# Kernel optimization log

Measured on AMD Instinct MI355X. Metric: run time of the kernel, lower is better.

The kernel has to match this reference:

```python
import jax, jax.numpy as jnp
import numpy as np

N = 8192          # total nodes in batch
D_IN = 64         # input feature dim
D_H = 64          # hidden dim
D_OUT = 10        # num classes
B = 64            # number of graphs (idx in [0, B))
NUM_ITERS = 5     # power iterations for rs-pool
VALUE_ALPHA = 1.0
EPS = 0.0         # GIN eps (train_eps=False)


def setup_inputs() -> dict:
    key = jax.random.key(0)
    ks = jax.random.split(key, 8)
    x_in = jax.random.normal(ks[0], (N, D_IN), dtype=jnp.float32)
    a = (jax.random.uniform(ks[1], (N, N)) < 0.005).astype(jnp.float32)
    adj = jnp.maximum(a, a.T)
    idx = (jnp.arange(N) // (N // B)).astype(jnp.int32)  # 64 graphs x 128 nodes
    s1 = 1.0 / np.sqrt(D_IN)
    s2 = 1.0 / np.sqrt(D_H)
    W1 = jax.random.uniform(ks[2], (D_IN, D_H), minval=-s1, maxval=s1, dtype=jnp.float32)
    b1 = jax.random.uniform(ks[3], (D_H,), minval=-s1, maxval=s1, dtype=jnp.float32)
    W2 = jax.random.uniform(ks[4], (D_H, D_H), minval=-s2, maxval=s2, dtype=jnp.float32)
    b2 = jax.random.uniform(ks[5], (D_H,), minval=-s2, maxval=s2, dtype=jnp.float32)
    Wl = jax.random.uniform(ks[6], (D_H, D_OUT), minval=-s2, maxval=s2, dtype=jnp.float32)
    bl = jax.random.uniform(ks[7], (D_OUT,), minval=-s2, maxval=s2, dtype=jnp.float32)
    return {"x_in": x_in, "adj": adj, "idx": idx,
            "W1": W1, "b1": b1, "W2": W2, "b2": b2, "Wl": Wl, "bl": bl}


def reference(x_in, adj, idx, W1, b1, W2, b2, Wl, bl):
    n = adj.shape[0]
    A = adj + jnp.eye(n, dtype=adj.dtype)  # self-loops added in forward
    # GINConv: aggregate (A@x + eps*x) then linear + ReLU
    h = jax.nn.relu((A @ x_in + EPS * x_in) @ W1 + b1)   # [N, D_H]
    h = jax.nn.relu((A @ h + EPS * h) @ W2 + b2)         # [N, D_H]

    seg = lambda v: jax.ops.segment_sum(v, idx, num_segments=B)

    # rs-pool: batched power iteration for dominant right singular vector per graph
    vec = seg(h)                                                   # [B, D_H]
    vec = vec / (jnp.linalg.norm(vec, axis=1, keepdims=True) + 1e-8)
    for _ in range(NUM_ITERS):
        y = jnp.sum(h * vec[idx], axis=1, keepdims=True)           # X_g @ v_g, per node
        vec = seg(y * h)                                           # X_g^T (X_g v_g)
        vec = vec / (jnp.linalg.norm(vec, axis=1, keepdims=True) + 1e-8)
    y = jnp.sum(h * vec[idx], axis=1)                              # [N]
    sv = jnp.sqrt(seg(y * y))                                      # ||X_g v_g|| per graph [B]
    pooled = vec * (sv / VALUE_ALPHA)[:, None]                     # [B, D_H]

    out = pooled @ Wl + bl                                         # [B, D_OUT]
    return jax.nn.log_softmax(out, axis=1)
```

## Files before the change

kernel.cpp:

```cpp
#include <hip/hip_runtime.h>
#include <math.h>

#define NN 8192
#define DH 64
#define DOUT 10
#define NG 64
#define NPG 128
#define NITER 5
#define CAP 192
#define NCHUNK (NN * NN / 256)
#define RPW 2

typedef float f32x4 __attribute__((ext_vector_type(4)));
typedef unsigned long long u64;
typedef u64 u64x2 __attribute__((ext_vector_type(2)));

__global__ __launch_bounds__(256) void scan_bitmap(
    const float* __restrict__ adj, u64* __restrict__ bmp)
{
    const int lane = threadIdx.x & 63;
    const int gw   = (blockIdx.x * 256 + threadIdx.x) >> 6;
    const int nw   = (gridDim.x * 256) >> 6;
    #pragma unroll 4
    for (int g = gw; g < NCHUNK; g += nw) {
        f32x4 a4 = *reinterpret_cast<const f32x4*>(adj + (size_t)g * 256 + lane * 4);
        u64 m0 = __ballot(a4.x != 0.0f);
        u64 m1 = __ballot(a4.y != 0.0f);
        u64 m2 = __ballot(a4.z != 0.0f);
        u64 m3 = __ballot(a4.w != 0.0f);
        u64 msel = (lane & 2) ? ((lane & 1) ? m3 : m2)
                              : ((lane & 1) ? m1 : m0);
        if (lane < 4) bmp[(size_t)g * 4 + lane] = msel;
    }
}

__global__ __launch_bounds__(256) void gin_layer(
    const float* __restrict__ x, const u64* __restrict__ bmp,
    const float* __restrict__ W, const float* __restrict__ bias,
    float* __restrict__ out)
{
    __shared__ float sW[DH * DH];
    __shared__ unsigned short sJ[4][CAP];

    for (int t = threadIdx.x; t < DH * DH; t += 256) sW[t] = W[t];
    __syncthreads();

    const int wave = threadIdx.x >> 6;
    const int lane = threadIdx.x & 63;

    float wreg[DH];
    #pragma unroll
    for (int k = 0; k < DH; ++k) wreg[k] = sW[k * DH + lane];
    const float bl_ = bias[lane];

    const int wgid = blockIdx.x * 4 + wave;

    for (int rr = 0; rr < RPW; ++rr) {
        const int row = wgid * RPW + rr;
        const u64* brow = bmp + (size_t)row * (NN / 64);

        u64x2 wp = *reinterpret_cast<const u64x2*>(brow + 2 * lane);
        u64 w0 = wp.x, w1 = wp.y;
        int cnt = __popcll(w0) + __popcll(w1);

        int p = cnt;
        #pragma unroll
        for (int off = 1; off < 64; off <<= 1) {
            int t = __shfl_up(p, off);
            if (lane >= off) p += t;
        }
        int pos  = p - cnt;
        int ctot = __shfl(p, 63);

        {
            int widx = 2 * lane;
            int base0 = (widx >> 2) * 256 + (widx & 3);
            while (w0) { int b = __ffsll(w0) - 1; w0 &= w0 - 1;
                         sJ[wave][pos++] = (unsigned short)(base0 + 4 * b); }
            int widx1 = 2 * lane + 1;
            int base1 = (widx1 >> 2) * 256 + (widx1 & 3);
            while (w1) { int b = __ffsll(w1) - 1; w1 &= w1 - 1;
                         sJ[wave][pos++] = (unsigned short)(base1 + 4 * b); }
        }

        float acc = x[row * DH + lane];
        #pragma unroll 4
        for (int e = 0; e < ctot; ++e) {
            int j = sJ[wave][e];
            acc += x[j * DH + lane];
        }

        float o = bl_;
        #pragma unroll
        for (int k = 0; k < DH; ++k)
            o = fmaf(__shfl(acc, k), wreg[k], o);
        out[row * DH + lane] = fmaxf(o, 0.0f);
    }
}

__global__ __launch_bounds__(256) void rspool_head(
    const float* __restrict__ h, const float* __restrict__ Wl,
    const float* __restrict__ bl, float* __restrict__ out)
{
    __shared__ float sX[NPG * 65];
    __shared__ float sY[NPG];
    __shared__ float sVec[DH];
    __shared__ float sPart[4][DH];
    __shared__ float sPooled[DH];
    __shared__ float sO[DOUT];

    const int g = blockIdx.x;
    const int d = threadIdx.x & 63;
    const int q = threadIdx.x >> 6;

    const float* hg = h + (size_t)g * NPG * DH;
    for (int t = threadIdx.x; t < NPG * DH; t += 256)
        sX[(t >> 6) * 65 + (t & 63)] = hg[t];
    __syncthreads();

    {
        float p = 0.0f;
        for (int i = q * 32; i < q * 32 + 32; ++i) p += sX[i * 65 + d];
        sPart[q][d] = p;
    }
    __syncthreads();
    if (threadIdx.x < 64) {
        float v = sPart[0][d] + sPart[1][d] + sPart[2][d] + sPart[3][d];
        float s = v * v;
        #pragma unroll
        for (int off = 32; off > 0; off >>= 1) s += __shfl_xor(s, off);
        sVec[d] = v / (sqrtf(s) + 1e-8f);
    }
    __syncthreads();

    for (int it = 0; it < NITER; ++it) {
        if (threadIdx.x < NPG) {
            int i = threadIdx.x;
            float yy = 0.0f;
            #pragma unroll
            for (int dd = 0; dd < DH; ++dd) yy += sX[i * 65 + dd] * sVec[dd];
            sY[i] = yy;
        }
        __syncthreads();
        {
            float p = 0.0f;
            for (int i = q * 32; i < q * 32 + 32; ++i) p += sY[i] * sX[i * 65 + d];
            sPart[q][d] = p;
        }
        __syncthreads();
        if (threadIdx.x < 64) {
            float v = sPart[0][d] + sPart[1][d] + sPart[2][d] + sPart[3][d];
            float s = v * v;
            #pragma unroll
            for (int off = 32; off > 0; off >>= 1) s += __shfl_xor(s, off);
            sVec[d] = v / (sqrtf(s) + 1e-8f);
        }
        __syncthreads();
    }

    if (threadIdx.x < NPG) {
        int i = threadIdx.x;
        float yy = 0.0f;
        #pragma unroll
        for (int dd = 0; dd < DH; ++dd) yy += sX[i * 65 + dd] * sVec[dd];
        sY[i] = yy;
    }
    __syncthreads();
    if (threadIdx.x < 64) {
        float s = sY[d] * sY[d] + sY[64 + d] * sY[64 + d];
        #pragma unroll
        for (int off = 32; off > 0; off >>= 1) s += __shfl_xor(s, off);
        float sv = sqrtf(s);
        sPooled[d] = sVec[d] * sv;
    }
    __syncthreads();

    if (threadIdx.x < DOUT) {
        int c = threadIdx.x;
        float o = bl[c];
        #pragma unroll
        for (int dd = 0; dd < DH; ++dd) o += sPooled[dd] * Wl[dd * DOUT + c];
        sO[c] = o;
    }
    __syncthreads();
    if (threadIdx.x < DOUT) {
        int c = threadIdx.x;
        float mx = -INFINITY;
        #pragma unroll
        for (int j = 0; j < DOUT; ++j) mx = fmaxf(mx, sO[j]);
        float se = 0.0f;
        #pragma unroll
        for (int j = 0; j < DOUT; ++j) se += expf(sO[j] - mx);
        out[g * DOUT + c] = sO[c] - mx - logf(se);
    }
}

extern "C" void kernel_launch(void* const* d_in, const int* in_sizes, int n_in,
                              void* d_out, int out_size, void* d_ws, size_t ws_size,
                              hipStream_t stream) {
    const float* x_in = (const float*)d_in[0];
    const float* adj  = (const float*)d_in[1];
    const float* W1 = (const float*)d_in[3];
    const float* b1 = (const float*)d_in[4];
    const float* W2 = (const float*)d_in[5];
    const float* b2 = (const float*)d_in[6];
    const float* Wl = (const float*)d_in[7];
    const float* bl = (const float*)d_in[8];
    float* out = (float*)d_out;

    char* ws = (char*)d_ws;
    float* h1 = (float*)ws;
    float* h2 = h1 + NN * DH;
    u64*   bmp = (u64*)(ws + 8 * 1024 * 1024);

    scan_bitmap<<<2048, 256, 0, stream>>>(adj, bmp);
    gin_layer<<<NN / (4 * RPW), 256, 0, stream>>>(x_in, bmp, W1, b1, h1);
    gin_layer<<<NN / (4 * RPW), 256, 0, stream>>>(h1, bmp, W2, b2, h2);
    rspool_head<<<NG, 256, 0, stream>>>(h2, Wl, bl, out);
}
```

Baseline: 100.3 us.

## Batch neighbor gathers, one row per wave, LDS-based GIN matvec

```diff
diff --git a/kernel.cpp b/kernel.cpp
--- a/kernel.cpp
+++ b/kernel.cpp
@@ -7,9 +7,8 @@
 #define NG 64
 #define NPG 128
 #define NITER 5
-#define CAP 192
+#define TPAD 160
 #define NCHUNK (NN * NN / 256)
-#define RPW 2
 
 typedef float f32x4 __attribute__((ext_vector_type(4)));
 typedef unsigned long long u64;
@@ -40,62 +39,62 @@
     float* __restrict__ out)
 {
     __shared__ float sW[DH * DH];
-    __shared__ unsigned short sJ[4][CAP];
+    __shared__ unsigned short sJ[4][TPAD];
+    __shared__ float sAccF[4][DH];
 
     for (int t = threadIdx.x; t < DH * DH; t += 256) sW[t] = W[t];
     __syncthreads();
 
     const int wave = threadIdx.x >> 6;
     const int lane = threadIdx.x & 63;
-
-    float wreg[DH];
+    const int row  = blockIdx.x * 4 + wave;
+
+    const u64* brow = bmp + (size_t)row * (NN / 64);
+    u64x2 wp = *reinterpret_cast<const u64x2*>(brow + 2 * lane);
+    u64 w0 = wp.x, w1 = wp.y;
+    int cnt = __popcll(w0) + __popcll(w1);
+
+    int p = cnt;
     #pragma unroll
-    for (int k = 0; k < DH; ++k) wreg[k] = sW[k * DH + lane];
-    const float bl_ = bias[lane];
-
-    const int wgid = blockIdx.x * 4 + wave;
-
-    for (int rr = 0; rr < RPW; ++rr) {
-        const int row = wgid * RPW + rr;
-        const u64* brow = bmp + (size_t)row * (NN / 64);
-
-        u64x2 wp = *reinterpret_cast<const u64x2*>(brow + 2 * lane);
-        u64 w0 = wp.x, w1 = wp.y;
-        int cnt = __popcll(w0) + __popcll(w1);
-
-        int p = cnt;
-        #pragma unroll
-        for (int off = 1; off < 64; off <<= 1) {
-            int t = __shfl_up(p, off);
-            if (lane >= off) p += t;
-        }
-        int pos  = p - cnt;
-        int ctot = __shfl(p, 63);
-
-        {
-            int widx = 2 * lane;
-            int base0 = (widx >> 2) * 256 + (widx & 3);
-            while (w0) { int b = __ffsll(w0) - 1; w0 &= w0 - 1;
-                         sJ[wave][pos++] = (unsigned short)(base0 + 4 * b); }
-            int widx1 = 2 * lane + 1;
-            int base1 = (widx1 >> 2) * 256 + (widx1 & 3);
-            while (w1) { int b = __ffsll(w1) - 1; w1 &= w1 - 1;
-                         sJ[wave][pos++] = (unsigned short)(base1 + 4 * b); }
-        }
-
-        float acc = x[row * DH + lane];
-        #pragma unroll 4
-        for (int e = 0; e < ctot; ++e) {
-            int j = sJ[wave][e];
-            acc += x[j * DH + lane];
-        }
-
-        float o = bl_;
-        #pragma unroll
-        for (int k = 0; k < DH; ++k)
-            o = fmaf(__shfl(acc, k), wreg[k], o);
-        out[row * DH + lane] = fmaxf(o, 0.0f);
-    }
+    for (int off = 1; off < 64; off <<= 1) {
+        int t = __shfl_up(p, off);
+        if (lane >= off) p += t;
+    }
+    int pos  = p - cnt;
+    int ctot = __shfl(p, 63);
+
+    {
+        int widx = 2 * lane;
+        int base0 = (widx >> 2) * 256 + (widx & 3);
+        while (w0) { int b = __ffsll(w0) - 1; w0 &= w0 - 1;
+                     sJ[wave][pos++] = (unsigned short)(base0 + 4 * b); }
+        int widx1 = 2 * lane + 1;
+        int base1 = (widx1 >> 2) * 256 + (widx1 & 3);
+        while (w1) { int b = __ffsll(w1) - 1; w1 &= w1 - 1;
+                     sJ[wave][pos++] = (unsigned short)(base1 + 4 * b); }
+    }
+    for (int e = ctot + lane; e < TPAD; e += 64) sJ[wave][e] = 0;
+
+    float acc = x[row * DH + lane];
+    const int tmax = (ctot + 15) & ~15;
+    #pragma unroll 1
+    for (int e0 = 0; e0 < tmax; e0 += 16) {
+        int jj[16];
+        float vv[16];
+        #pragma unroll
+        for (int s = 0; s < 16; ++s) jj[s] = sJ[wave][e0 + s];
+        #pragma unroll
+        for (int s = 0; s < 16; ++s) vv[s] = x[jj[s] * DH + lane];
+        #pragma unroll
+        for (int s = 0; s < 16; ++s)
+            acc += (e0 + s < ctot) ? vv[s] : 0.0f;
+    }
+
+    sAccF[wave][lane] = acc;
+    float o = bias[lane];
+    #pragma unroll
+    for (int k = 0; k < DH; ++k) o += sAccF[wave][k] * sW[k * DH + lane];
+    out[row * DH + lane] = fmaxf(o, 0.0f);
 }
 
 __global__ __launch_bounds__(256) void rspool_head(
@@ -214,7 +213,7 @@
     u64*   bmp = (u64*)(ws + 8 * 1024 * 1024);
 
     scan_bitmap<<<2048, 256, 0, stream>>>(adj, bmp);
-    gin_layer<<<NN / (4 * RPW), 256, 0, stream>>>(x_in, bmp, W1, b1, h1);
-    gin_layer<<<NN / (4 * RPW), 256, 0, stream>>>(h1, bmp, W2, b2, h2);
+    gin_layer<<<NN / 4, 256, 0, stream>>>(x_in, bmp, W1, b1, h1);
+    gin_layer<<<NN / 4, 256, 0, stream>>>(h1, bmp, W2, b2, h2);
     rspool_head<<<NG, 256, 0, stream>>>(h2, Wl, bl, out);
 }
```

Result: faster. 89.01 us (-11.3%).
